# Optimization experiments

Hardware: AMD Instinct MI355X
Metric: run time of the kernel (lower is better)

Reference implementation:

```python
import jax, jax.numpy as jnp
import numpy as np

B, L, E = 256, 500, 300  # bsz, max_doc_len, word_embed_dim
KS = [3, 5, 7]           # filters_size


def setup_inputs() -> dict:
    key = jax.random.key(0)
    ks = jax.random.split(key, 1 + 2 * len(KS))
    inp = {"x": jax.random.normal(ks[0], (B, L, E), jnp.float32)}
    i = 1
    for k in KS:
        # PyTorch Conv2d default init scale ~ 1/sqrt(fan_in)
        inp[f"aw{k}"] = jax.random.normal(ks[i], (k, E), jnp.float32) / np.sqrt(k * E).astype(np.float32); i += 1
        inp[f"ab{k}"] = jnp.zeros((1,), jnp.float32)
        inp[f"cw{k}"] = jax.random.normal(ks[i], (E,), jnp.float32) / np.sqrt(E).astype(np.float32); i += 1
        inp[f"cb{k}"] = jnpp = jnp.zeros((1,), jnp.float32)
    return inp


def _branch(x, aw, ab, cw, cb):
    # x: (B, L, E); aw: (k, E); cw: (E,)
    k = aw.shape[0]
    p = (k - 1) // 2
    x4 = x[:, None, :, :]            # NCHW: (B, 1, L, E)
    w4 = aw[None, None, :, :]        # OIHW: (1, 1, k, E)
    s = jax.lax.conv_general_dilated(x4, w4, window_strides=(1, 1),
                                     padding=((p, p), (0, 0)))  # (B, 1, L, 1)
    score = jax.nn.sigmoid(s + ab[0])[:, 0, :, :]               # (B, L, 1)
    gated = x * score                                           # broadcast over E
    # Conv2d(1,1,(1,E)) == per-timestep dot product over E
    return jnp.tanh(jnp.einsum('ble,e->bl', gated, cw) + cb[0])  # (B, L)


def reference(x, aw3, ab3, cw3, cb3, aw5, ab5, cw5, cb5, aw7, ab7, cw7, cb7):
    return (_branch(x, aw3, ab3, cw3, cb3),
            _branch(x, aw5, ab5, cw5, cb5),
            _branch(x, aw7, ab7, cw7, cb7))
```

## Files before the change

kernel.cpp:

```cpp
#include <hip/hip_runtime.h>
#include <math.h>

#define BB 256
#define LL 500
#define EE 300
#define NROWS (BB * LL)
#define NJ 18
#define NC 75
#define CB 5
#define NB 15
#define DR 256
#define TOUT 250
#define XB4 (DR * CB)

__global__ __launch_bounds__(256) void fused_kernel(
    const float* __restrict__ x,
    const float* __restrict__ aw3, const float* __restrict__ ab3,
    const float* __restrict__ cw3, const float* __restrict__ cb3,
    const float* __restrict__ aw5, const float* __restrict__ ab5,
    const float* __restrict__ cw5, const float* __restrict__ cb5,
    const float* __restrict__ aw7, const float* __restrict__ ab7,
    const float* __restrict__ cw7, const float* __restrict__ cb7,
    float* __restrict__ out)
{
    __shared__ float4 wlds[NJ * NC];
    __shared__ float4 xbuf[2][XB4];
    float* dlds = (float*)&xbuf[0][0];

    const int tid = threadIdx.x;
    const int b   = blockIdx.x >> 1;
    const int t   = blockIdx.x & 1;
    const int l0  = t * TOUT - 3;

    const float4* xp[5];
#pragma unroll
    for (int q = 0; q < 5; ++q) {
        const int L   = q * 256 + tid;
        const int row = L / CB;
        const int cc  = L - row * CB;
        int g = l0 + row;
        g = g < 0 ? 0 : (g >= LL ? LL - 1 : g);
        xp[q] = (const float4*)(x + ((size_t)b * LL + g) * EE) + cc;
    }

    float4 xn[5];
#pragma unroll
    for (int q = 0; q < 5; ++q) xn[q] = xp[q][0];

    {
        const float4* s3a = (const float4*)aw3;
        const float4* s3c = (const float4*)cw3;
        const float4* s5a = (const float4*)aw5;
        const float4* s5c = (const float4*)cw5;
        const float4* s7a = (const float4*)aw7;
        const float4* s7c = (const float4*)cw7;
        for (int i = tid; i < 225; i += 256) wlds[i]        = s3a[i];
        for (int i = tid; i < 75;  i += 256) wlds[225 + i]  = s3c[i];
        for (int i = tid; i < 375; i += 256) wlds[300 + i]  = s5a[i];
        for (int i = tid; i < 75;  i += 256) wlds[675 + i]  = s5c[i];
        for (int i = tid; i < 525; i += 256) wlds[750 + i]  = s7a[i];
        for (int i = tid; i < 75;  i += 256) wlds[1275 + i] = s7c[i];
    }

#pragma unroll
    for (int q = 0; q < 5; ++q) xbuf[0][q * 256 + tid] = xn[q];

    __syncthreads();

    const int wav   = tid >> 6;
    const int lane  = tid & 63;
    const int dbase = (wav >> 1) * 9;
    const int rbase = (wav & 1) * 128 + lane;

    float vf0, vf1;
    { const int g0 = l0 + rbase;      vf0 = (g0 >= 0 && g0 < LL) ? 1.0f : 0.0f; }
    { const int g1 = l0 + rbase + 64; vf1 = (g1 >= 0 && g1 < LL) ? 1.0f : 0.0f; }

    float acc[9][2];
#pragma unroll
    for (int dd = 0; dd < 9; ++dd) { acc[dd][0] = 0.0f; acc[dd][1] = 0.0f; }

#pragma unroll 1
    for (int s = 0; s < NB; ++s) {
        if (s < NB - 1) {
#pragma unroll
            for (int q = 0; q < 5; ++q) { xp[q] += CB; xn[q] = xp[q][0]; }
        }

        const float4* xb = &xbuf[s & 1][rbase * CB];
        const float4* wb = &wlds[dbase * NC + s * CB];

#pragma unroll
        for (int cc = 0; cc < CB; ++cc) {
            const float4 x0 = xb[cc];
            const float4 x1 = xb[64 * CB + cc];
#pragma unroll
            for (int dd = 0; dd < 9; ++dd) {
                const float4 w = wb[dd * NC + cc];
                acc[dd][0] = fmaf(x0.w, w.w, fmaf(x0.z, w.z, fmaf(x0.y, w.y, fmaf(x0.x, w.x, acc[dd][0]))));
                acc[dd][1] = fmaf(x1.w, w.w, fmaf(x1.z, w.z, fmaf(x1.y, w.y, fmaf(x1.x, w.x, acc[dd][1]))));
            }
        }

        if (s < NB - 1) {
#pragma unroll
            for (int q = 0; q < 5; ++q) xbuf[(s + 1) & 1][q * 256 + tid] = xn[q];
        }
        __syncthreads();
    }

#pragma unroll
    for (int dd = 0; dd < 9; ++dd) {
        dlds[rbase * (NJ + 1) + dbase + dd]        = acc[dd][0] * vf0;
        dlds[(rbase + 64) * (NJ + 1) + dbase + dd] = acc[dd][1] * vf1;
    }
    __syncthreads();

    if (tid < TOUT) {
        const int c = tid + 3;
        const int r = b * LL + t * TOUT + tid;
        {
            float pre = 0.0f;
#pragma unroll
            for (int tp = 0; tp < 3; ++tp) pre += dlds[(c + tp - 1) * (NJ + 1) + tp];
            const float sg = 1.0f / (1.0f + expf(-(pre + ab3[0])));
            out[r] = tanhf(sg * dlds[c * (NJ + 1) + 3] + cb3[0]);
        }
        {
            float pre = 0.0f;
#pragma unroll
            for (int tp = 0; tp < 5; ++tp) pre += dlds[(c + tp - 2) * (NJ + 1) + 4 + tp];
            const float sg = 1.0f / (1.0f + expf(-(pre + ab5[0])));
            out[NROWS + r] = tanhf(sg * dlds[c * (NJ + 1) + 9] + cb5[0]);
        }
        {
            float pre = 0.0f;
#pragma unroll
            for (int tp = 0; tp < 7; ++tp) pre += dlds[(c + tp - 3) * (NJ + 1) + 10 + tp];
            const float sg = 1.0f / (1.0f + expf(-(pre + ab7[0])));
            out[2 * NROWS + r] = tanhf(sg * dlds[c * (NJ + 1) + 17] + cb7[0]);
        }
    }
}

extern "C" void kernel_launch(void* const* d_in, const int* in_sizes, int n_in,
                              void* d_out, int out_size, void* d_ws, size_t ws_size,
                              hipStream_t stream) {
    const float* x   = (const float*)d_in[0];
    const float* aw3 = (const float*)d_in[1];
    const float* ab3 = (const float*)d_in[2];
    const float* cw3 = (const float*)d_in[3];
    const float* cb3 = (const float*)d_in[4];
    const float* aw5 = (const float*)d_in[5];
    const float* ab5 = (const float*)d_in[6];
    const float* cw5 = (const float*)d_in[7];
    const float* cb5 = (const float*)d_in[8];
    const float* aw7 = (const float*)d_in[9];
    const float* ab7 = (const float*)d_in[10];
    const float* cw7 = (const float*)d_in[11];
    const float* cb7 = (const float*)d_in[12];

    float* out = (float*)d_out;

    fused_kernel<<<BB * 2, 256, 0, stream>>>(
        x, aw3, ab3, cw3, cb3, aw5, ab5, cw5, cb5, aw7, ab7, cw7, cb7, out);
}
```

Before: 292.3 us.

## Restructure into per-wave jobs with transposed weights read via scalar broadcast

Result: no change. 292.2 us (-0.0%).

```diff
diff --git a/kernel.cpp b/kernel.cpp
--- a/kernel.cpp
+++ b/kernel.cpp
@@ -5,140 +5,158 @@
 #define LL 500
 #define EE 300
 #define NROWS (BB * LL)
-#define NJ 18
-#define NC 75
-#define CB 5
-#define NB 15
-#define DR 256
-#define TOUT 250
-#define XB4 (DR * CB)
+#define ND 18
+#define WSTR 20
+#define KT 16
+#define NTILES 19
+#define KPAD (NTILES * KT)
+#define WR 64
+#define OPW 58
+#define JPB 9
+#define XSTR 17
+#define DSTR 19
+
+
+__global__ void wt_transpose(
+    const float* __restrict__ aw3, const float* __restrict__ aw5,
+    const float* __restrict__ aw7, const float* __restrict__ cw3,
+    const float* __restrict__ cw5, const float* __restrict__ cw7,
+    float* __restrict__ wt)
+{
+    const int idx = blockIdx.x * 256 + threadIdx.x;
+    if (idx >= KPAD * WSTR) return;
+    const int k = idx / WSTR;
+    const int d = idx - k * WSTR;
+    float v = 0.0f;
+    if (k < EE && d < ND) {
+        if      (d < 3)  v = aw3[d * EE + k];
+        else if (d == 3) v = cw3[k];
+        else if (d < 9)  v = aw5[(d - 4) * EE + k];
+        else if (d == 9) v = cw5[k];
+        else if (d < 17) v = aw7[(d - 10) * EE + k];
+        else             v = cw7[k];
+    }
+    wt[idx] = v;
+}
 
 __global__ __launch_bounds__(256) void fused_kernel(
-    const float* __restrict__ x,
-    const float* __restrict__ aw3, const float* __restrict__ ab3,
-    const float* __restrict__ cw3, const float* __restrict__ cb3,
-    const float* __restrict__ aw5, const float* __restrict__ ab5,
-    const float* __restrict__ cw5, const float* __restrict__ cb5,
-    const float* __restrict__ aw7, const float* __restrict__ ab7,
-    const float* __restrict__ cw7, const float* __restrict__ cb7,
+    const float* __restrict__ x, const float* __restrict__ wt,
+    const float* __restrict__ ab3, const float* __restrict__ cb3,
+    const float* __restrict__ ab5, const float* __restrict__ cb5,
+    const float* __restrict__ ab7, const float* __restrict__ cb7,
     float* __restrict__ out)
 {
-    __shared__ float4 wlds[NJ * NC];
-    __shared__ float4 xbuf[2][XB4];
-    float* dlds = (float*)&xbuf[0][0];
+    __shared__ float xlds[4][2][WR * XSTR];
 
-    const int tid = threadIdx.x;
-    const int b   = blockIdx.x >> 1;
-    const int t   = blockIdx.x & 1;
-    const int l0  = t * TOUT - 3;
+    const int tid   = threadIdx.x;
+    const int wave  = tid >> 6;
+    const int lane  = tid & 63;
+    const int job   = blockIdx.x * 4 + wave;
+    const int batch = job / JPB;
+    const int t     = job - batch * JPB;
+    const int l0    = t * OPW - 3;
 
-    const float4* xp[5];
+    const float* xbb = x + (size_t)batch * LL * EE;
+    float* xw = &xlds[wave][0][0];
+
+    const int srow = lane >> 2;
+    const int sc   = lane & 3;
+
+    const float* srp[4];
 #pragma unroll
-    for (int q = 0; q < 5; ++q) {
-        const int L   = q * 256 + tid;
-        const int row = L / CB;
-        const int cc  = L - row * CB;
-        int g = l0 + row;
-        g = g < 0 ? 0 : (g >= LL ? LL - 1 : g);
-        xp[q] = (const float4*)(x + ((size_t)b * LL + g) * EE) + cc;
+    for (int p = 0; p < 4; ++p) {
+        int l = l0 + srow + p * 16;
+        l = l < 0 ? 0 : (l >= LL ? LL - 1 : l);
+        srp[p] = xbb + (size_t)l * EE;
     }
 
-    float4 xn[5];
+    float4 g[4];
 #pragma unroll
-    for (int q = 0; q < 5; ++q) xn[q] = xp[q][0];
-
-    {
-        const float4* s3a = (const float4*)aw3;
-        const float4* s3c = (const float4*)cw3;
-        const float4* s5a = (const float4*)aw5;
-        const float4* s5c = (const float4*)cw5;
-        const float4* s7a = (const float4*)aw7;
-        const float4* s7c = (const float4*)cw7;
-        for (int i = tid; i < 225; i += 256) wlds[i]        = s3a[i];
-        for (int i = tid; i < 75;  i += 256) wlds[225 + i]  = s3c[i];
-        for (int i = tid; i < 375; i += 256) wlds[300 + i]  = s5a[i];
-        for (int i = tid; i < 75;  i += 256) wlds[675 + i]  = s5c[i];
-        for (int i = tid; i < 525; i += 256) wlds[750 + i]  = s7a[i];
-        for (int i = tid; i < 75;  i += 256) wlds[1275 + i] = s7c[i];
+    for (int p = 0; p < 4; ++p) g[p] = *(const float4*)(srp[p] + sc * 4);
+#pragma unroll
+    for (int p = 0; p < 4; ++p) {
+        const int base = (srow + p * 16) * XSTR + sc * 4;
+        xw[base + 0] = g[p].x; xw[base + 1] = g[p].y;
+        xw[base + 2] = g[p].z; xw[base + 3] = g[p].w;
     }
 
+    float acc[ND];
 #pragma unroll
-    for (int q = 0; q < 5; ++q) xbuf[0][q * 256 + tid] = xn[q];
-
-    __syncthreads();
-
-    const int wav   = tid >> 6;
-    const int lane  = tid & 63;
-    const int dbase = (wav >> 1) * 9;
-    const int rbase = (wav & 1) * 128 + lane;
-
-    float vf0, vf1;
-    { const int g0 = l0 + rbase;      vf0 = (g0 >= 0 && g0 < LL) ? 1.0f : 0.0f; }
-    { const int g1 = l0 + rbase + 64; vf1 = (g1 >= 0 && g1 < LL) ? 1.0f : 0.0f; }
-
-    float acc[9][2];
-#pragma unroll
-    for (int dd = 0; dd < 9; ++dd) { acc[dd][0] = 0.0f; acc[dd][1] = 0.0f; }
+    for (int d = 0; d < ND; ++d) acc[d] = 0.0f;
 
 #pragma unroll 1
-    for (int s = 0; s < NB; ++s) {
-        if (s < NB - 1) {
+    for (int tt = 0; tt < NTILES; ++tt) {
+        const int nt = tt + 1;
+        if (nt < NTILES) {
+            const int k0 = nt * KT;
+            const bool tail = (nt == NTILES - 1) && (sc == 3);
 #pragma unroll
-            for (int q = 0; q < 5; ++q) { xp[q] += CB; xn[q] = xp[q][0]; }
-        }
-
-        const float4* xb = &xbuf[s & 1][rbase * CB];
-        const float4* wb = &wlds[dbase * NC + s * CB];
-
-#pragma unroll
-        for (int cc = 0; cc < CB; ++cc) {
-            const float4 x0 = xb[cc];
-            const float4 x1 = xb[64 * CB + cc];
-#pragma unroll
-            for (int dd = 0; dd < 9; ++dd) {
-                const float4 w = wb[dd * NC + cc];
-                acc[dd][0] = fmaf(x0.w, w.w, fmaf(x0.z, w.z, fmaf(x0.y, w.y, fmaf(x0.x, w.x, acc[dd][0]))));
-                acc[dd][1] = fmaf(x1.w, w.w, fmaf(x1.z, w.z, fmaf(x1.y, w.y, fmaf(x1.x, w.x, acc[dd][1]))));
+            for (int p = 0; p < 4; ++p) {
+                if (tail) { g[p].x = 0.f; g[p].y = 0.f; g[p].z = 0.f; g[p].w = 0.f; }
+                else      { g[p] = *(const float4*)(srp[p] + k0 + sc * 4); }
             }
         }
 
-        if (s < NB - 1) {
+        const float* xb   = xw + (tt & 1) * (WR * XSTR) + lane * XSTR;
+        const float* wrow = wt + tt * KT * WSTR;
+
+        float xv[KT];
 #pragma unroll
-            for (int q = 0; q < 5; ++q) xbuf[(s + 1) & 1][q * 256 + tid] = xn[q];
+        for (int kk = 0; kk < KT; ++kk) xv[kk] = xb[kk];
+#pragma unroll
+        for (int kk = 0; kk < KT; ++kk) {
+#pragma unroll
+            for (int d = 0; d < ND; ++d)
+                acc[d] = fmaf(wrow[kk * WSTR + d], xv[kk], acc[d]);
         }
-        __syncthreads();
+
+        if (nt < NTILES) {
+            float* xn = xw + (nt & 1) * (WR * XSTR);
+#pragma unroll
+            for (int p = 0; p < 4; ++p) {
+                const int base = (srow + p * 16) * XSTR + sc * 4;
+                xn[base + 0] = g[p].x; xn[base + 1] = g[p].y;
+                xn[base + 2] = g[p].z; xn[base + 3] = g[p].w;
+            }
+        }
     }
 
+    {
+        const int lg = l0 + lane;
+        const float vf = (lg >= 0 && lg < LL) ? 1.0f : 0.0f;
 #pragma unroll
-    for (int dd = 0; dd < 9; ++dd) {
-        dlds[rbase * (NJ + 1) + dbase + dd]        = acc[dd][0] * vf0;
-        dlds[(rbase + 64) * (NJ + 1) + dbase + dd] = acc[dd][1] * vf1;
+        for (int d = 0; d < ND; ++d) xw[lane * DSTR + d] = acc[d] * vf;
     }
-    __syncthreads();
+    asm volatile("s_waitcnt lgkmcnt(0)" ::: "memory");
 
-    if (tid < TOUT) {
-        const int c = tid + 3;
-        const int r = b * LL + t * TOUT + tid;
-        {
-            float pre = 0.0f;
+    if (lane >= 3 && lane < 3 + OPW) {
+        const int lo = l0 + lane;
+        if (lo < LL) {
+            const int r = batch * LL + lo;
+            const float cen3 = xw[lane * DSTR + 3];
+            const float cen5 = xw[lane * DSTR + 9];
+            const float cen7 = xw[lane * DSTR + 17];
+            {
+                float pre = 0.0f;
 #pragma unroll
-            for (int tp = 0; tp < 3; ++tp) pre += dlds[(c + tp - 1) * (NJ + 1) + tp];
-            const float sg = 1.0f / (1.0f + expf(-(pre + ab3[0])));
-            out[r] = tanhf(sg * dlds[c * (NJ + 1) + 3] + cb3[0]);
-        }
-        {
-            float pre = 0.0f;
+                for (int tp = 0; tp < 3; ++tp) pre += xw[(lane + tp - 1) * DSTR + tp];
+                const float s = 1.0f / (1.0f + expf(-(pre + ab3[0])));
+                out[r] = tanhf(s * cen3 + cb3[0]);
+            }
+            {
+                float pre = 0.0f;
 #pragma unroll
-            for (int tp = 0; tp < 5; ++tp) pre += dlds[(c + tp - 2) * (NJ + 1) + 4 + tp];
-            const float sg = 1.0f / (1.0f + expf(-(pre + ab5[0])));
-            out[NROWS + r] = tanhf(sg * dlds[c * (NJ + 1) + 9] + cb5[0]);
-        }
-        {
-            float pre = 0.0f;
+                for (int tp = 0; tp < 5; ++tp) pre += xw[(lane + tp - 2) * DSTR + 4 + tp];
+                const float s = 1.0f / (1.0f + expf(-(pre + ab5[0])));
+                out[NROWS + r] = tanhf(s * cen5 + cb5[0]);
+            }
+            {
+                float pre = 0.0f;
 #pragma unroll
-            for (int tp = 0; tp < 7; ++tp) pre += dlds[(c + tp - 3) * (NJ + 1) + 10 + tp];
-            const float sg = 1.0f / (1.0f + expf(-(pre + ab7[0])));
-            out[2 * NROWS + r] = tanhf(sg * dlds[c * (NJ + 1) + 17] + cb7[0]);
+                for (int tp = 0; tp < 7; ++tp) pre += xw[(lane + tp - 3) * DSTR + 10 + tp];
+                const float s = 1.0f / (1.0f + expf(-(pre + ab7[0])));
+                out[2 * NROWS + r] = tanhf(s * cen7 + cb7[0]);
+            }
         }
     }
 }
@@ -160,8 +178,12 @@
     const float* cw7 = (const float*)d_in[11];
     const float* cb7 = (const float*)d_in[12];
 
+    float* wt  = (float*)d_ws;
     float* out = (float*)d_out;
 
-    fused_kernel<<<BB * 2, 256, 0, stream>>>(
-        x, aw3, ab3, cw3, cb3, aw5, ab5, cw5, cb5, aw7, ab7, cw7, cb7, out);
+    wt_transpose<<<(KPAD * WSTR + 255) / 256, 256, 0, stream>>>(
+        aw3, aw5, aw7, cw3, cw5, cw7, wt);
+
+    fused_kernel<<<(BB * JPB) / 4, 256, 0, stream>>>(
+        x, wt, ab3, cb3, ab5, cb5, ab7, cb7, out);
 }
```
